# Kernel tuning notes

Hardware: AMD Instinct MI355X
Metric: run time of the kernel (lower is better)

Reference implementation:

```python
import jax, jax.numpy as jnp
import numpy as np

N = 100000
E = 1000000
C = 64      # hidden_channels
H = 4       # heads
O = C // H  # out channels per head
NEG_SLOPE = 0.2


def setup_inputs() -> dict:
    key = jax.random.key(0)
    ks = jax.random.split(key, 14)
    x = jax.random.normal(ks[0], (N, C), dtype=jnp.float32)
    edge_index = jax.random.randint(ks[1], (2, E), 0, N, dtype=jnp.int64)
    s = 1.0 / np.sqrt(C)
    params = {}
    for l in range(3):
        params[f"Wl{l+1}"] = jax.random.normal(ks[2 + 4 * l], (C, H * O), dtype=jnp.float32) * s
        params[f"Wr{l+1}"] = jax.random.normal(ks[3 + 4 * l], (C, H * O), dtype=jnp.float32) * s
        params[f"a{l+1}"] = jax.random.normal(ks[4 + 4 * l], (H, O), dtype=jnp.float32) * s
        params[f"b{l+1}"] = jnp.zeros((H * O,), dtype=jnp.float32)
    return {"x": x, "edge_index": edge_index, **params}


def _gatv2_layer(x, src, dst, Wl, Wr, a, b):
    # x: [N, C]; src/dst: [E]
    xl = (x @ Wl).reshape(N, H, O)  # source-side transform
    xr = (x @ Wr).reshape(N, H, O)  # target-side transform
    s = jax.nn.leaky_relu(xl[src] + xr[dst], NEG_SLOPE)     # [E, H, O]
    e = jnp.einsum("eho,ho->eh", s, a)                       # [E, H] logits
    # segment softmax over incoming edges of each target node
    m = jax.ops.segment_max(e, dst, num_segments=N)          # [N, H]
    ex = jnp.exp(e - m[dst])
    denom = jax.ops.segment_sum(ex, dst, num_segments=N)     # [N, H]
    alpha = ex / (denom[dst] + 1e-16)                        # [E, H]
    out = jax.ops.segment_sum(xl[src] * alpha[:, :, None], dst, num_segments=N)
    return out.reshape(N, H * O) + b


def reference(x, edge_index, Wl1, Wr1, a1, b1, Wl2, Wr2, a2, b2, Wl3, Wr3, a3, b3):
    src, dst = edge_index[0], edge_index[1]
    h = jax.nn.relu(_gatv2_layer(x, src, dst, Wl1, Wr1, a1, b1))
    h = jax.nn.relu(_gatv2_layer(h, src, dst, Wl2, Wr2, a2, b2))
    h = _gatv2_layer(h, src, dst, Wl3, Wr3, a3, b3)
    return h
```

## Files before the change

kernel.cpp:

```cpp
#include <hip/hip_runtime.h>
#include <math.h>

#define SLOPE 0.2f
#define LOG2E 1.4426950408889634f

#define DPP_ADD(x, ctrl) \
    ((x) + __int_as_float(__builtin_amdgcn_update_dpp( \
        0, __float_as_int(x), (ctrl), 0xF, 0xF, true)))


#define NPB 256
#define EPB 8192
#define MAXBK 2048

__global__ __launch_bounds__(256) void kH1(const int* __restrict__ ei,
                                           int* __restrict__ hist,
                                           int E, int nbk, int nblkE) {
    __shared__ int h[MAXBK];
    int t = threadIdx.x, b = blockIdx.x;
    for (int i = t; i < nbk; i += 256) h[i] = 0;
    __syncthreads();
    int e0 = b * EPB, e1 = min(e0 + EPB, E);
    for (int e = e0 + t; e < e1; e += 256)
        atomicAdd(&h[ei[E + e] >> 8], 1);
    __syncthreads();
    for (int i = t; i < nbk; i += 256)
        hist[i * nblkE + b] = h[i];
}

__global__ __launch_bounds__(256) void kH2(const int* __restrict__ ei,
                                           const int* __restrict__ hs,
                                           int* __restrict__ pairs,
                                           int E, int nbk, int nblkE) {
    __shared__ int soff[MAXBK];
    int t = threadIdx.x, b = blockIdx.x;
    for (int i = t; i < nbk; i += 256) soff[i] = hs[i * nblkE + b];
    __syncthreads();
    int e0 = b * EPB, e1 = min(e0 + EPB, E);
    for (int e = e0 + t; e < e1; e += 256) {
        int s = ei[e], d = ei[E + e];
        int slot = atomicAdd(&soff[d >> 8], 1);
        pairs[slot] = (s << 8) | (d & (NPB - 1));
    }
}

__global__ __launch_bounds__(256) void kB3(const int* __restrict__ hs,
                                           const int* __restrict__ pairs,
                                           int* __restrict__ deg,
                                           int E, int nbk, int nblkE, int n) {
    __shared__ int sdeg[NPB];
    int t = threadIdx.x, b = blockIdx.x;
    sdeg[t] = 0;
    __syncthreads();
    int s0 = hs[b * nblkE];
    int s1 = (b + 1 < nbk) ? hs[(b + 1) * nblkE] : E;
    for (int i = s0 + t; i < s1; i += 256)
        atomicAdd(&sdeg[pairs[i] & (NPB - 1)], 1);
    __syncthreads();
    int node = b * NPB + t;
    if (node < n) deg[node] = sdeg[t];
}

__global__ __launch_bounds__(256) void kB4(const int* __restrict__ hs,
                                           const int* __restrict__ pairs,
                                           const int* __restrict__ rp,
                                           int* __restrict__ col,
                                           int E, int nbk, int nblkE, int n) {
    __shared__ int scur[NPB];
    int t = threadIdx.x, b = blockIdx.x;
    int node = b * NPB + t;
    scur[t] = (node < n) ? rp[node] : 0;
    __syncthreads();
    int s0 = hs[b * nblkE];
    int s1 = (b + 1 < nbk) ? hs[(b + 1) * nblkE] : E;
    for (int i = s0 + t; i < s1; i += 256) {
        int p = pairs[i];
        int slot = atomicAdd(&scur[p & (NPB - 1)], 1);
        col[slot] = p & ~(NPB - 1);
    }
}


__global__ __launch_bounds__(256) void k_scan1(const int* __restrict__ deg,
                                               int* __restrict__ rp,
                                               int* __restrict__ blk, int n,
                                               int pad4) {
    __shared__ int sd[256];
    int t = threadIdx.x;
    int base = blockIdx.x * 1024 + t * 4;
    int v0 = 0, v1 = 0, v2 = 0, v3 = 0;
    if (base + 0 < n) v0 = deg[base + 0];
    if (base + 1 < n) v1 = deg[base + 1];
    if (base + 2 < n) v2 = deg[base + 2];
    if (base + 3 < n) v3 = deg[base + 3];
    if (pad4) {
        v0 = (v0 + 3) & ~3; v1 = (v1 + 3) & ~3;
        v2 = (v2 + 3) & ~3; v3 = (v3 + 3) & ~3;
    }
    int s = v0 + v1 + v2 + v3;
    sd[t] = s;
    __syncthreads();
    for (int off = 1; off < 256; off <<= 1) {
        int x = (t >= off) ? sd[t - off] : 0;
        __syncthreads();
        sd[t] += x;
        __syncthreads();
    }
    int ex = sd[t] - s;
    if (t == 255) blk[blockIdx.x] = sd[255];
    if (base + 0 < n) rp[base + 0] = ex; ex += v0;
    if (base + 1 < n) rp[base + 1] = ex; ex += v1;
    if (base + 2 < n) rp[base + 2] = ex; ex += v2;
    if (base + 3 < n) rp[base + 3] = ex;
}

__global__ __launch_bounds__(256) void k_scan2(int* __restrict__ blk, int nblk) {
    __shared__ int sd[256];
    int t = threadIdx.x;
    int v = (t < nblk) ? blk[t] : 0;
    sd[t] = v;
    __syncthreads();
    for (int off = 1; off < 256; off <<= 1) {
        int x = (t >= off) ? sd[t - off] : 0;
        __syncthreads();
        sd[t] += x;
        __syncthreads();
    }
    if (t < nblk) blk[t] = sd[t] - v;
}

__global__ __launch_bounds__(256) void k_scan3(int* __restrict__ rp,
                                               const int* __restrict__ blk,
                                               int n) {
    int t = threadIdx.x;
    int base = blockIdx.x * 1024 + t * 4;
    int off = blk[blockIdx.x];
    #pragma unroll
    for (int i = 0; i < 4; i++) {
        int idx = base + i;
        if (idx < n) rp[idx] += off;
    }
}


__global__ __launch_bounds__(256) void k_gemm(const float* __restrict__ in,
                                              const float* __restrict__ Wl,
                                              const float* __restrict__ Wr,
                                              float* __restrict__ xl,
                                              float* __restrict__ xr, int n) {
    __shared__ float4 sW[64 * 32];
    __shared__ float  sx[64 * 68];

    int t = threadIdx.x;
    int base = blockIdx.x * 64;

    float4 xs[4];
    int xrow[4], xkq[4];
    #pragma unroll
    for (int s = 0; s < 4; s++) {
        int i = t + 256 * s;
        int row = i >> 4, kq = i & 15;
        int g = base + row;
        if (g > n - 1) g = n - 1;
        xs[s] = *(const float4*)(in + (size_t)g * 64 + kq * 4);
        xrow[s] = row; xkq[s] = kq;
    }
    for (int i = t; i < 2048; i += 256) {
        int k = i >> 5, jg = i & 31;
        const float* src = (jg < 16) ? (Wl + k * 64 + jg * 4)
                                     : (Wr + k * 64 + (jg - 16) * 4);
        sW[i] = *(const float4*)src;
    }
    #pragma unroll
    for (int s = 0; s < 4; s++)
        *(float4*)(sx + xrow[s] * 68 + xkq[s] * 4) = xs[s];
    __syncthreads();

    int rt = t & 15;
    int ct = t >> 4;
    const float* sxp = sx + rt * 68;

    float4 acc[4][2];
    #pragma unroll
    for (int r = 0; r < 4; r++)
        #pragma unroll
        for (int j = 0; j < 2; j++) acc[r][j] = make_float4(0.f, 0.f, 0.f, 0.f);

    #pragma unroll 1
    for (int k0 = 0; k0 < 64; k0 += 4) {
        float4 xv[4];
        #pragma unroll
        for (int r = 0; r < 4; r++)
            xv[r] = *(const float4*)(sxp + r * (16 * 68) + k0);
        #pragma unroll
        for (int kk = 0; kk < 4; kk++) {
            float4 w0 = sW[(k0 + kk) * 32 + ct * 2 + 0];
            float4 w1 = sW[(k0 + kk) * 32 + ct * 2 + 1];
            #pragma unroll
            for (int r = 0; r < 4; r++) {
                float xk = (kk == 0) ? xv[r].x : (kk == 1) ? xv[r].y
                         : (kk == 2) ? xv[r].z : xv[r].w;
                acc[r][0].x += xk * w0.x;
                acc[r][0].y += xk * w0.y;
                acc[r][0].z += xk * w0.z;
                acc[r][0].w += xk * w0.w;
                acc[r][1].x += xk * w1.x;
                acc[r][1].y += xk * w1.y;
                acc[r][1].z += xk * w1.z;
                acc[r][1].w += xk * w1.w;
            }
        }
    }

    float* outh = (ct < 8) ? xl : xr;
    int cq = (ct & 7) * 8;
    #pragma unroll
    for (int r = 0; r < 4; r++) {
        int g = base + rt + 16 * r;
        if (g < n) {
            float* dst = outh + (size_t)g * 64 + cq;
            *(float4*)(dst + 0) = acc[r][0];
            *(float4*)(dst + 4) = acc[r][1];
        }
    }
}


__global__ __launch_bounds__(256) void k_node(const float* __restrict__ xl,
                                              const float* __restrict__ xr,
                                              const int* __restrict__ rp,
                                              const int* __restrict__ deg,
                                              const int* __restrict__ col,
                                              const float* __restrict__ A,
                                              const float* __restrict__ Bv,
                                              float* __restrict__ outp,
                                              int n, int relu) {
    int lane = threadIdx.x & 63;
    int node = blockIdx.x * 4 + (threadIdx.x >> 6);
    if (node >= n) return;
    unsigned lane4 = (unsigned)lane * 4u;

    float xr_d = xr[(size_t)node * 64 + lane];
    float a_l = A[lane] * LOG2E;
    float b_l = Bv[lane];

    int start = rp[node];
    int d = deg[node];
    int nb = (d + 7) >> 3;
    const int* cp = col + start;
    const char* xlb = (const char*)xl;

    float den = 0.f, acc = 0.f;

    auto batch = [&](const float (&v)[8], int valid) {
        float p[8];
        #pragma unroll
        for (int j = 0; j < 8; j++) {
            float s = v[j] + xr_d;
            s = fmaxf(s, SLOPE * s);
            float q = s * a_l;
            q = DPP_ADD(q, 0xB1);
            q = DPP_ADD(q, 0x4E);
            q = DPP_ADD(q, 0x141);
            q = DPP_ADD(q, 0x140);
            p[j] = q;
        }
        if (valid < 8) {
            #pragma unroll
            for (int j = 0; j < 8; j++)
                if (j >= valid) p[j] = -INFINITY;
        }
        #pragma unroll
        for (int j = 0; j < 8; j++) {
            float w = exp2f(p[j]);
            den += w;
            acc += w * v[j];
        }
    };

    float v[8];
    if (nb > 0) {
        int c[8];
        *(int4*)(c + 0) = *(const int4*)(cp + 0);
        *(int4*)(c + 4) = *(const int4*)(cp + 4);
        #pragma unroll
        for (int j = 0; j < 8; j++)
            v[j] = *(const float*)(xlb + ((unsigned)c[j] + lane4));
    }

    #pragma unroll 1
    for (int b = 0; b < nb - 1; b++) {
        int cN[8];
        float vN[8];
        const int* q = cp + (b + 1) * 8;
        *(int4*)(cN + 0) = *(const int4*)(q + 0);
        *(int4*)(cN + 4) = *(const int4*)(q + 4);
        #pragma unroll
        for (int j = 0; j < 8; j++)
            vN[j] = *(const float*)(xlb + ((unsigned)cN[j] + lane4));

        batch(v, 8);

        #pragma unroll
        for (int j = 0; j < 8; j++) v[j] = vN[j];
    }

    if (nb > 0) {
        batch(v, d - (nb - 1) * 8);
    }

    float o = acc / (den + 1e-16f) + b_l;
    if (relu) o = fmaxf(o, 0.f);
    outp[(size_t)node * 64 + lane] = o;
}


extern "C" void kernel_launch(void* const* d_in, const int* in_sizes, int n_in,
                              void* d_out, int out_size, void* d_ws, size_t ws_size,
                              hipStream_t stream) {
    const float* x = (const float*)d_in[0];
    const int* ei = (const int*)d_in[1];
    int N = in_sizes[0] / 64;
    int E = in_sizes[1] / 2;

    const float* Wl[3] = {(const float*)d_in[2], (const float*)d_in[6], (const float*)d_in[10]};
    const float* Wr[3] = {(const float*)d_in[3], (const float*)d_in[7], (const float*)d_in[11]};
    const float* Av[3] = {(const float*)d_in[4], (const float*)d_in[8], (const float*)d_in[12]};
    const float* Bv[3] = {(const float*)d_in[5], (const float*)d_in[9], (const float*)d_in[13]};

    char* w = (char*)d_ws;
    auto carve = [&](size_t bytes) {
        void* p = (void*)w;
        w += (bytes + 255) & ~(size_t)255;
        return p;
    };
    int NBK    = (N + NPB - 1) / NPB;
    int NBLK_E = (E + EPB - 1) / EPB;
    size_t histN = (size_t)NBK * NBLK_E;
    size_t colN = (size_t)E + 3 * (size_t)N + 64;
    float* xl    = (float*)carve((size_t)N * 64 * 4);
    float* xr    = (float*)carve((size_t)N * 64 * 4);
    float* h     = (float*)carve((size_t)N * 64 * 4);
    int*   rp    = (int*)carve((size_t)N * 4);
    int*   deg   = (int*)carve((size_t)N * 4);
    int*   col   = (int*)carve(colN * 4);
    int*   pairs = (int*)carve((size_t)E * 4);
    int*   hist  = (int*)carve(histN * 4);
    int*   hs    = (int*)carve(histN * 4);
    int*   blk   = (int*)carve(256 * 4);
    int*   blkB  = (int*)carve(256 * 4);

    int nblk1024 = (N + 1023) / 1024;
    int nblkH1024 = (int)((histN + 1023) / 1024);
    int gemm_grid = (N + 63) / 64;
    int node_grid = (N + 3) / 4;

    hipMemsetAsync(col, 0, colN * 4, stream);

    kH1<<<NBLK_E, 256, 0, stream>>>(ei, hist, E, NBK, NBLK_E);
    k_scan1<<<nblkH1024, 256, 0, stream>>>(hist, hs, blkB, (int)histN, 0);
    k_scan2<<<1, 256, 0, stream>>>(blkB, nblkH1024);
    k_scan3<<<nblkH1024, 256, 0, stream>>>(hs, blkB, (int)histN);
    kH2<<<NBLK_E, 256, 0, stream>>>(ei, hs, pairs, E, NBK, NBLK_E);

    kB3<<<NBK, 256, 0, stream>>>(hs, pairs, deg, E, NBK, NBLK_E, N);
    k_scan1<<<nblk1024, 256, 0, stream>>>(deg, rp, blk, N, 1);
    k_scan2<<<1, 256, 0, stream>>>(blk, nblk1024);
    k_scan3<<<nblk1024, 256, 0, stream>>>(rp, blk, N);
    kB4<<<NBK, 256, 0, stream>>>(hs, pairs, rp, col, E, NBK, NBLK_E, N);

    const float* in_l = x;
    for (int l = 0; l < 3; l++) {
        float* out_l = (l == 2) ? (float*)d_out : h;
        int relu = (l < 2) ? 1 : 0;
        k_gemm<<<gemm_grid, 256, 0, stream>>>(in_l, Wl[l], Wr[l], xl, xr, N);
        k_node<<<node_grid, 256, 0, stream>>>(xl, xr, rp, deg, col, Av[l], Bv[l],
                                              out_l, N, relu);
        in_l = h;
    }
}
```

Measured before the change: 400.4 us.

## Fuse CSR degree scan into bucket kernels and use native exp2 in node kernel

Result: faster. 379.5 us (-5.2%).

```diff
diff --git a/kernel.cpp b/kernel.cpp
--- a/kernel.cpp
+++ b/kernel.cpp
@@ -46,9 +46,10 @@
 
 __global__ __launch_bounds__(256) void kB3(const int* __restrict__ hs,
                                            const int* __restrict__ pairs,
-                                           int* __restrict__ deg,
-                                           int E, int nbk, int nblkE, int n) {
+                                           int* __restrict__ btot,
+                                           int E, int nbk, int nblkE) {
     __shared__ int sdeg[NPB];
+    __shared__ int red[256];
     int t = threadIdx.x, b = blockIdx.x;
     sdeg[t] = 0;
     __syncthreads();
@@ -57,25 +58,75 @@
     for (int i = s0 + t; i < s1; i += 256)
         atomicAdd(&sdeg[pairs[i] & (NPB - 1)], 1);
     __syncthreads();
-    int node = b * NPB + t;
-    if (node < n) deg[node] = sdeg[t];
+    red[t] = (sdeg[t] + 3) & ~3;
+    __syncthreads();
+    for (int off = 128; off; off >>= 1) {
+        if (t < off) red[t] += red[t + off];
+        __syncthreads();
+    }
+    if (t == 0) btot[b] = red[0];
+}
+
+__global__ __launch_bounds__(256) void kscanB(const int* __restrict__ btot,
+                                              int* __restrict__ bbase, int nbk) {
+    __shared__ int sd[256];
+    __shared__ int carry;
+    int t = threadIdx.x;
+    if (t == 0) carry = 0;
+    __syncthreads();
+    for (int base = 0; base < nbk; base += 256) {
+        int v = (base + t < nbk) ? btot[base + t] : 0;
+        sd[t] = v;
+        __syncthreads();
+        for (int off = 1; off < 256; off <<= 1) {
+            int x = (t >= off) ? sd[t - off] : 0;
+            __syncthreads();
+            sd[t] += x;
+            __syncthreads();
+        }
+        if (base + t < nbk) bbase[base + t] = sd[t] - v + carry;
+        __syncthreads();
+        if (t == 255) carry += sd[255];
+        __syncthreads();
+    }
 }
 
 __global__ __launch_bounds__(256) void kB4(const int* __restrict__ hs,
                                            const int* __restrict__ pairs,
-                                           const int* __restrict__ rp,
+                                           const int* __restrict__ bbase,
+                                           int* __restrict__ rp,
+                                           int* __restrict__ deg,
                                            int* __restrict__ col,
                                            int E, int nbk, int nblkE, int n) {
-    __shared__ int scur[NPB];
+    __shared__ int sdeg[NPB];
+    __shared__ int spfx[NPB];
     int t = threadIdx.x, b = blockIdx.x;
-    int node = b * NPB + t;
-    scur[t] = (node < n) ? rp[node] : 0;
+    sdeg[t] = 0;
     __syncthreads();
     int s0 = hs[b * nblkE];
     int s1 = (b + 1 < nbk) ? hs[(b + 1) * nblkE] : E;
+    for (int i = s0 + t; i < s1; i += 256)
+        atomicAdd(&sdeg[pairs[i] & (NPB - 1)], 1);
+    __syncthreads();
+    int cnt = sdeg[t];
+    int pv = (cnt + 3) & ~3;
+    spfx[t] = pv;
+    __syncthreads();
+    for (int off = 1; off < 256; off <<= 1) {
+        int x = (t >= off) ? spfx[t - off] : 0;
+        __syncthreads();
+        spfx[t] += x;
+        __syncthreads();
+    }
+    int rpt = bbase[b] + spfx[t] - pv;
+    int node = b * NPB + t;
+    if (node < n) { rp[node] = rpt; deg[node] = cnt; }
+    __syncthreads();
+    sdeg[t] = rpt;
+    __syncthreads();
     for (int i = s0 + t; i < s1; i += 256) {
         int p = pairs[i];
-        int slot = atomicAdd(&scur[p & (NPB - 1)], 1);
+        int slot = atomicAdd(&sdeg[p & (NPB - 1)], 1);
         col[slot] = p & ~(NPB - 1);
     }
 }
@@ -83,8 +134,7 @@
 
 __global__ __launch_bounds__(256) void k_scan1(const int* __restrict__ deg,
                                                int* __restrict__ rp,
-                                               int* __restrict__ blk, int n,
-                                               int pad4) {
+                                               int* __restrict__ blk, int n) {
     __shared__ int sd[256];
     int t = threadIdx.x;
     int base = blockIdx.x * 1024 + t * 4;
@@ -93,10 +143,6 @@
     if (base + 1 < n) v1 = deg[base + 1];
     if (base + 2 < n) v2 = deg[base + 2];
     if (base + 3 < n) v3 = deg[base + 3];
-    if (pad4) {
-        v0 = (v0 + 3) & ~3; v1 = (v1 + 3) & ~3;
-        v2 = (v2 + 3) & ~3; v3 = (v3 + 3) & ~3;
-    }
     int s = v0 + v1 + v2 + v3;
     sd[t] = s;
     __syncthreads();
@@ -236,7 +282,7 @@
                                               float* __restrict__ outp,
                                               int n, int relu) {
     int lane = threadIdx.x & 63;
-    int node = blockIdx.x * 4 + (threadIdx.x >> 6);
+    int node = __builtin_amdgcn_readfirstlane(blockIdx.x * 4 + (threadIdx.x >> 6));
     if (node >= n) return;
     unsigned lane4 = (unsigned)lane * 4u;
 
@@ -272,7 +318,7 @@
         }
         #pragma unroll
         for (int j = 0; j < 8; j++) {
-            float w = exp2f(p[j]);
+            float w = __builtin_amdgcn_exp2f(p[j]);
             den += w;
             acc += w * v[j];
         }
@@ -347,10 +393,10 @@
     int*   pairs = (int*)carve((size_t)E * 4);
     int*   hist  = (int*)carve(histN * 4);
     int*   hs    = (int*)carve(histN * 4);
-    int*   blk   = (int*)carve(256 * 4);
+    int*   btot  = (int*)carve((size_t)NBK * 4);
+    int*   bbase = (int*)carve((size_t)NBK * 4);
     int*   blkB  = (int*)carve(256 * 4);
 
-    int nblk1024 = (N + 1023) / 1024;
     int nblkH1024 = (int)((histN + 1023) / 1024);
     int gemm_grid = (N + 63) / 64;
     int node_grid = (N + 3) / 4;
@@ -358,16 +404,14 @@
     hipMemsetAsync(col, 0, colN * 4, stream);
 
     kH1<<<NBLK_E, 256, 0, stream>>>(ei, hist, E, NBK, NBLK_E);
-    k_scan1<<<nblkH1024, 256, 0, stream>>>(hist, hs, blkB, (int)histN, 0);
+    k_scan1<<<nblkH1024, 256, 0, stream>>>(hist, hs, blkB, (int)histN);
     k_scan2<<<1, 256, 0, stream>>>(blkB, nblkH1024);
     k_scan3<<<nblkH1024, 256, 0, stream>>>(hs, blkB, (int)histN);
     kH2<<<NBLK_E, 256, 0, stream>>>(ei, hs, pairs, E, NBK, NBLK_E);
 
-    kB3<<<NBK, 256, 0, stream>>>(hs, pairs, deg, E, NBK, NBLK_E, N);
-    k_scan1<<<nblk1024, 256, 0, stream>>>(deg, rp, blk, N, 1);
-    k_scan2<<<1, 256, 0, stream>>>(blk, nblk1024);
-    k_scan3<<<nblk1024, 256, 0, stream>>>(rp, blk, N);
-    kB4<<<NBK, 256, 0, stream>>>(hs, pairs, rp, col, E, NBK, NBLK_E, N);
+    kB3<<<NBK, 256, 0, stream>>>(hs, pairs, btot, E, NBK, NBLK_E);
+    kscanB<<<1, 256, 0, stream>>>(btot, bbase, NBK);
+    kB4<<<NBK, 256, 0, stream>>>(hs, pairs, bbase, rp, deg, col, E, NBK, NBLK_E, N);
 
     const float* in_l = x;
     for (int l = 0; l < 3; l++) {
```
